# Kernel tuning notes

Measured on AMD Instinct MI355X. Metric: run time of the kernel, lower is better.

Reference implementation:

```python
import jax, jax.numpy as jnp
import numpy as np

N = 100000
E = 1600000
F_IN = 128
H = 128
C = 2


def setup_inputs() -> dict:
    key = jax.random.key(0)
    ks = jax.random.split(key, 12)
    s = lambda fan_in: 1.0 / np.sqrt(fan_in)
    inp = {
        "x": jax.random.normal(ks[0], (N, F_IN), dtype=jnp.float32),
        "edge_index": jax.random.randint(ks[1], (2, E), 0, N, dtype=jnp.int32),
        "edge_weight": jax.random.uniform(ks[2], (E,), dtype=jnp.float32),
        # first_lin: features_num -> hidden
        "W_first": jax.random.uniform(ks[3], (F_IN, H), minval=-s(F_IN), maxval=s(F_IN)),
        "b_first": jnp.zeros((H,), jnp.float32),
        # GRUCell (torch layout: [3*H, H] for ih and hh)
        "W_ih": jax.random.uniform(ks[4], (3 * H, H), minval=-s(H), maxval=s(H)),
        "b_ih": jax.random.uniform(ks[5], (3 * H,), minval=-s(H), maxval=s(H)),
        "W_hh": jax.random.uniform(ks[6], (3 * H, H), minval=-s(H), maxval=s(H)),
        "b_hh": jax.random.uniform(ks[7], (3 * H,), minval=-s(H), maxval=s(H)),
        # lin1: hidden -> hidden
        "W_lin1": jax.random.uniform(ks[8], (H, H), minval=-s(H), maxval=s(H)),
        "b_lin1": jnp.zeros((H,), jnp.float32),
        # out: hidden -> num_class
        "W_out": jax.random.uniform(ks[9], (H, C), minval=-s(H), maxval=s(H)),
        "b_out": jnp.zeros((C,), jnp.float32),
    }
    return inp


def _gated_conv(x, edge_index, edge_weight):
    # gather source node features, scale by edge weight, scatter-add to dst
    src, dst = edge_index[0], edge_index[1]
    msg = x[src] * edge_weight[:, None]           # [E, H]
    return jax.ops.segment_sum(msg, dst, num_segments=N)  # [N, H]


def _gru_cell(inp, hid, W_ih, b_ih, W_hh, b_hh):
    gi = inp @ W_ih.T + b_ih                      # [N, 3H]
    gh = hid @ W_hh.T + b_hh                      # [N, 3H]
    i_r, i_z, i_n = jnp.split(gi, 3, axis=-1)
    h_r, h_z, h_n = jnp.split(gh, 3, axis=-1)
    r = jax.nn.sigmoid(i_r + h_r)
    z = jax.nn.sigmoid(i_z + h_z)
    n = jnp.tanh(i_n + r * h_n)
    return (1.0 - z) * n + z * hid


def reference(x, edge_index, edge_weight, W_first, b_first, W_ih, b_ih,
              W_hh, b_hh, W_lin1, b_lin1, W_out, b_out):
    x = x @ W_first + b_first                     # [N, H] (dropout: eval mode no-op)
    h = x
    x = _gated_conv(x, edge_index, edge_weight)
    x = _gru_cell(x, h, W_ih, b_ih, W_hh, b_hh)
    x = x @ W_lin1 + b_lin1
    x = _gated_conv(x, edge_index, edge_weight)
    x = _gru_cell(x, h, W_ih, b_ih, W_hh, b_hh)
    logits = x @ W_out + b_out                    # [N, C]
    return jax.nn.log_softmax(logits, axis=-1)
```

## Files before the change

### kernel.cpp

```cpp
#include <hip/hip_runtime.h>
#include <hip/hip_bf16.h>

#define H 128
#define SCAN_T 256
#define SCAN_I 8
#define SCAN_CHUNK (SCAN_T * SCAN_I)

typedef __bf16 bf16_t;
typedef __attribute__((ext_vector_type(2))) __bf16 bf16x2;
typedef __attribute__((ext_vector_type(8))) __bf16 bf16x8;
typedef __attribute__((ext_vector_type(4))) float f32x4;

static_assert(sizeof(bf16x8) == 16, "bf16x8 must be 16 bytes");

__device__ inline bf16x8 load_a_frag_f32(const float* __restrict__ A, int row, int koff) {
    const float4* p = (const float4*)(A + (size_t)row * H + koff);
    float4 v0 = p[0], v1 = p[1];
    bf16x8 r;
    r[0] = (bf16_t)v0.x; r[1] = (bf16_t)v0.y; r[2] = (bf16_t)v0.z; r[3] = (bf16_t)v0.w;
    r[4] = (bf16_t)v1.x; r[5] = (bf16_t)v1.y; r[6] = (bf16_t)v1.z; r[7] = (bf16_t)v1.w;
    return r;
}

__global__ void prep_weights(const float* __restrict__ Wf,  const float* __restrict__ Wih,
                             const float* __restrict__ Whh, const float* __restrict__ Wl1,
                             bf16_t* __restrict__ wfT, bf16_t* __restrict__ wih,
                             bf16_t* __restrict__ whh, bf16_t* __restrict__ wl1T) {
    int i = blockIdx.x * blockDim.x + threadIdx.x;
    if (i < 128 * 128) {
        int c = i >> 7, k = i & 127;
        wfT[i]  = (bf16_t)Wf[k * 128 + c];
        wl1T[i] = (bf16_t)Wl1[k * 128 + c];
    }
    if (i < 384 * 128) {
        wih[i] = (bf16_t)Wih[i];
        whh[i] = (bf16_t)Whh[i];
    }
}

__global__ void hist_kernel(const int* __restrict__ ei, int* __restrict__ deg, int nE) {
    int e = blockIdx.x * blockDim.x + threadIdx.x;
    if (e < nE) atomicAdd(&deg[ei[nE + e]], 1);
}

__global__ __launch_bounds__(SCAN_T) void scan1_kernel(
    const int* __restrict__ deg, int* __restrict__ rowptr, int* __restrict__ bsum, int n) {
    __shared__ int s[SCAN_T];
    int base = blockIdx.x * SCAN_CHUNK + threadIdx.x * SCAN_I;
    int v[SCAN_I];
    int sum = 0;
    for (int j = 0; j < SCAN_I; ++j) {
        int idx = base + j;
        v[j] = (idx < n) ? deg[idx] : 0;
        sum += v[j];
    }
    s[threadIdx.x] = sum;
    __syncthreads();
    for (int off = 1; off < SCAN_T; off <<= 1) {
        int t = (threadIdx.x >= off) ? s[threadIdx.x - off] : 0;
        __syncthreads();
        s[threadIdx.x] += t;
        __syncthreads();
    }
    int run = s[threadIdx.x] - sum;
    for (int j = 0; j < SCAN_I; ++j) {
        int idx = base + j;
        if (idx < n) rowptr[idx] = run;
        run += v[j];
    }
    if (threadIdx.x == SCAN_T - 1) bsum[blockIdx.x] = s[SCAN_T - 1];
}

__global__ __launch_bounds__(SCAN_T) void scan2_kernel(int* __restrict__ bsum, int nb) {
    __shared__ int s[SCAN_T];
    int v = (threadIdx.x < nb) ? bsum[threadIdx.x] : 0;
    s[threadIdx.x] = v;
    __syncthreads();
    for (int off = 1; off < SCAN_T; off <<= 1) {
        int t = (threadIdx.x >= off) ? s[threadIdx.x - off] : 0;
        __syncthreads();
        s[threadIdx.x] += t;
        __syncthreads();
    }
    if (threadIdx.x < nb) bsum[threadIdx.x] = s[threadIdx.x] - v;
}

__global__ void scan3_kernel(int* __restrict__ rowptr, int* __restrict__ cursor,
                             const int* __restrict__ bsum, int n, int nE) {
    int idx = blockIdx.x * blockDim.x + threadIdx.x;
    if (idx < n) {
        int val = rowptr[idx] + bsum[idx / SCAN_CHUNK];
        rowptr[idx] = val;
        cursor[idx] = val;
    }
    if (idx == 0) rowptr[n] = nE;
}

__global__ __launch_bounds__(256) void scatter_kernel(
    const int* __restrict__ ei, const float* __restrict__ ew,
    int* __restrict__ cursor, int2* __restrict__ srcw, int nE, int n) {
    int r = blockIdx.x & 7;
    int nslice = n >> 3;
    int lo = r * nslice;
    int hi = (r == 7) ? n : lo + nslice;
    int chunk = blockIdx.x >> 3;
    int nchunk = gridDim.x >> 3;
    for (int e = chunk * 256 + threadIdx.x; e < nE; e += nchunk * 256) {
        int dst = ei[nE + e];
        if (dst >= lo && dst < hi) {
            int pos = atomicAdd(&cursor[dst], 1);
            srcw[pos] = make_int2(ei[e], __float_as_int(ew[e]));
        }
    }
}

__device__ inline void conv_fma(float* acc, uint4 u, float w) {
    acc[0] += __uint_as_float(u.x << 16) * w;
    acc[1] += __uint_as_float(u.x & 0xffff0000u) * w;
    acc[2] += __uint_as_float(u.y << 16) * w;
    acc[3] += __uint_as_float(u.y & 0xffff0000u) * w;
    acc[4] += __uint_as_float(u.z << 16) * w;
    acc[5] += __uint_as_float(u.z & 0xffff0000u) * w;
    acc[6] += __uint_as_float(u.w << 16) * w;
    acc[7] += __uint_as_float(u.w & 0xffff0000u) * w;
}

__global__ __launch_bounds__(256) void conv_csr_kernel(
    const bf16_t* __restrict__ xb, const int* __restrict__ rowptr,
    const int2* __restrict__ srcw, bf16_t* __restrict__ agg, int n) {
    int lane = threadIdx.x & 63;
    int d = (blockIdx.x * blockDim.x + threadIdx.x) >> 6;
    if (d >= n) return;
    int q = lane >> 4;
    int l = lane & 15;
    int beg = rowptr[d], end = rowptr[d + 1];

    float acc[8];
    #pragma unroll
    for (int i = 0; i < 8; ++i) acc[i] = 0.f;

    int e = beg + q;
    for (; e + 4 < end; e += 8) {
        int2 sw0 = srcw[e];
        int2 sw1 = srcw[e + 4];
        uint4 u0 = *(const uint4*)(xb + (size_t)sw0.x * H + l * 8);
        uint4 u1 = *(const uint4*)(xb + (size_t)sw1.x * H + l * 8);
        conv_fma(acc, u0, __int_as_float(sw0.y));
        conv_fma(acc, u1, __int_as_float(sw1.y));
    }
    if (e < end) {
        int2 sw = srcw[e];
        uint4 u = *(const uint4*)(xb + (size_t)sw.x * H + l * 8);
        conv_fma(acc, u, __int_as_float(sw.y));
    }

    #pragma unroll
    for (int i = 0; i < 8; ++i) {
        acc[i] += __shfl_xor(acc[i], 16);
        acc[i] += __shfl_xor(acc[i], 32);
    }
    if (q == 0) {
        bf16x8 r;
        #pragma unroll
        for (int i = 0; i < 8; ++i) r[i] = (bf16_t)acc[i];
        *(bf16x8*)(agg + (size_t)d * H + l * 8) = r;
    }
}


__global__ __launch_bounds__(256) void lin_first_kernel(
    const float* __restrict__ A, const bf16_t* __restrict__ Bt,
    const float* __restrict__ bias, bf16_t* __restrict__ outb, int n) {
    __shared__ __align__(16) unsigned char wlds[32768];
    int tid = threadIdx.x;
    int wid = tid >> 6, lane = tid & 63;
    int r0 = (blockIdx.x * 4 + wid) * 32;
    int lrow = lane & 15, lq = lane >> 4, lk8 = lq * 8;

    #pragma unroll
    for (int i = 0; i < 8; ++i) {
        int g = i * 256 + tid;
        int row = g >> 4, seg = g & 15;
        uint4 v = *(const uint4*)(Bt + row * 128 + seg * 8);
        *(uint4*)(&wlds[row * 256 + ((seg * 16) ^ ((row & 7) << 4))]) = v;
    }

    bf16x8 a[2][4];
    for (int rt = 0; rt < 2; ++rt) {
        int row = r0 + rt * 16 + lrow;
        if (row >= n) row = n - 1;
        for (int t = 0; t < 4; ++t) a[rt][t] = load_a_frag_f32(A, row, t * 32 + lk8);
    }
    __syncthreads();

    for (int ct = 0; ct < 8; ++ct) {
        int c0 = ct * 16;
        f32x4 acc0 = {0.f, 0.f, 0.f, 0.f}, acc1 = {0.f, 0.f, 0.f, 0.f};
        int rbase = (c0 + lrow) * 256;
        int sw = (lrow & 7) << 4;
        #pragma unroll
        for (int t = 0; t < 4; ++t) {
            bf16x8 b = *(const bf16x8*)(&wlds[rbase + ((t * 64 + lq * 16) ^ sw)]);
            acc0 = __builtin_amdgcn_mfma_f32_16x16x32_bf16(a[0][t], b, acc0, 0, 0, 0);
            acc1 = __builtin_amdgcn_mfma_f32_16x16x32_bf16(a[1][t], b, acc1, 0, 0, 0);
        }
        int col = c0 + lrow;
        float bv = bias[col];
        for (int r = 0; r < 4; ++r) {
            int row0 = r0 + lq * 4 + r;
            if (row0 < n) outb[(size_t)row0 * H + col] = (bf16_t)(acc0[r] + bv);
            int row1 = row0 + 16;
            if (row1 < n) outb[(size_t)row1 * H + col] = (bf16_t)(acc1[r] + bv);
        }
    }
}

__global__ __launch_bounds__(256) void lin_mid_kernel(
    const bf16_t* __restrict__ A, const bf16_t* __restrict__ Bt,
    const float* __restrict__ bias, bf16_t* __restrict__ out, int n) {
    __shared__ __align__(16) unsigned char wlds[32768];
    int tid = threadIdx.x;
    int wid = tid >> 6, lane = tid & 63;
    int r0 = (blockIdx.x * 4 + wid) * 32;
    int lrow = lane & 15, lq = lane >> 4, lk8 = lq * 8;

    #pragma unroll
    for (int i = 0; i < 8; ++i) {
        int g = i * 256 + tid;
        int row = g >> 4, seg = g & 15;
        uint4 v = *(const uint4*)(Bt + row * 128 + seg * 8);
        *(uint4*)(&wlds[row * 256 + ((seg * 16) ^ ((row & 7) << 4))]) = v;
    }

    bf16x8 a[2][4];
    for (int rt = 0; rt < 2; ++rt) {
        int row = r0 + rt * 16 + lrow;
        if (row >= n) row = n - 1;
        for (int t = 0; t < 4; ++t)
            a[rt][t] = *(const bf16x8*)(A + (size_t)row * H + t * 32 + lk8);
    }
    __syncthreads();

    for (int ct = 0; ct < 8; ++ct) {
        int c0 = ct * 16;
        f32x4 acc0 = {0.f, 0.f, 0.f, 0.f}, acc1 = {0.f, 0.f, 0.f, 0.f};
        int rbase = (c0 + lrow) * 256;
        int sw = (lrow & 7) << 4;
        #pragma unroll
        for (int t = 0; t < 4; ++t) {
            bf16x8 b = *(const bf16x8*)(&wlds[rbase + ((t * 64 + lq * 16) ^ sw)]);
            acc0 = __builtin_amdgcn_mfma_f32_16x16x32_bf16(a[0][t], b, acc0, 0, 0, 0);
            acc1 = __builtin_amdgcn_mfma_f32_16x16x32_bf16(a[1][t], b, acc1, 0, 0, 0);
        }
        int col = c0 + lrow;
        float bv = bias[col];
        for (int r = 0; r < 4; ++r) {
            int row0 = r0 + lq * 4 + r;
            if (row0 < n) out[(size_t)row0 * H + col] = (bf16_t)(acc0[r] + bv);
            int row1 = row0 + 16;
            if (row1 < n) out[(size_t)row1 * H + col] = (bf16_t)(acc1[r] + bv);
        }
    }
}

template<bool LOGITS>
__global__ __launch_bounds__(256) void gru_kernel(
    const bf16_t* __restrict__ inp, const bf16_t* __restrict__ hidb,
    const bf16_t* __restrict__ Wih, const bf16_t* __restrict__ Whh,
    const float* __restrict__ bih, const float* __restrict__ bhh,
    bf16_t* __restrict__ out, const float* __restrict__ Wo,
    float* __restrict__ pl, int n) {
    __shared__ __align__(16) unsigned char wlds[12 * 4096];
    int tid = threadIdx.x;
    int wid = tid >> 6, lane = tid & 63;
    int cg = blockIdx.x & 3;
    int rb = blockIdx.x >> 2;
    int rstride = gridDim.x >> 2;
    int lrow = lane & 15, lq = lane >> 4, lk8 = lq * 8;

    int srow = tid >> 4, sseg = tid & 15;
    int s_src = srow * 128 + sseg * 8;
    int s_lds = srow * 256 + ((sseg * 16) ^ ((srow & 7) << 4));
    #pragma unroll
    for (int p = 0; p < 2; ++p) {
        #pragma unroll
        for (int s = 0; s < 3; ++s) {
            *(uint4*)(&wlds[(p * 6 + s) * 4096 + s_lds]) =
                *(const uint4*)(Wih + (size_t)(s * 128 + cg * 32 + p * 16) * 128 + s_src);
            *(uint4*)(&wlds[(p * 6 + 3 + s) * 4096 + s_lds]) =
                *(const uint4*)(Whh + (size_t)(s * 128 + cg * 32 + p * 16) * 128 + s_src);
        }
    }
    __syncthreads();

    int colA = cg * 32 + lrow, colB = colA + 16;
    float birA = bih[colA], bizA = bih[128 + colA], binA = bih[256 + colA];
    float bhrA = bhh[colA], bhzA = bhh[128 + colA], bhnA = bhh[256 + colA];
    float birB = bih[colB], bizB = bih[128 + colB], binB = bih[256 + colB];
    float bhrB = bhh[colB], bhzB = bhh[128 + colB], bhnB = bhh[256 + colB];
    float w0A = 0.f, w1A = 0.f, w0B = 0.f, w1B = 0.f;
    if (LOGITS) {
        float2 wa = *(const float2*)(Wo + colA * 2); w0A = wa.x; w1A = wa.y;
        float2 wb = *(const float2*)(Wo + colB * 2); w0B = wb.x; w1B = wb.y;
    }
    bf16x8 bidA, bidB;
    #pragma unroll
    for (int j = 0; j < 8; ++j) {
        bidA[j] = (bf16_t)((lq == (lrow >> 3) && j == (lrow & 7)) ? 1.f : 0.f);
        int ix = 16 + lrow;
        bidB[j] = (bf16_t)((lq == (ix >> 3) && j == (ix & 7)) ? 1.f : 0.f);
    }
    int rbase = lrow * 256;
    int swz = (lrow & 7) << 4;

    int nrt = (n + 63) >> 6;
    for (int rbi = rb; rbi < nrt; rbi += rstride) {
        int r0 = rbi * 64 + wid * 16;
        int rowl = r0 + lrow;
        if (rowl >= n) rowl = n - 1;
        bf16x8 ai[4], ah[4];
        #pragma unroll
        for (int t = 0; t < 4; ++t) {
            ai[t] = *(const bf16x8*)(inp  + (size_t)rowl * H + t * 32 + lk8);
            ah[t] = *(const bf16x8*)(hidb + (size_t)rowl * H + t * 32 + lk8);
        }
        float s0[4], s1[4];
        if (LOGITS) {
            #pragma unroll
            for (int r = 0; r < 4; ++r) { s0[r] = 0.f; s1[r] = 0.f; }
        }

        #pragma unroll
        for (int p = 0; p < 2; ++p) {
            f32x4 air = {0.f,0.f,0.f,0.f}, aiz = {0.f,0.f,0.f,0.f}, ain = {0.f,0.f,0.f,0.f};
            f32x4 ahr = {0.f,0.f,0.f,0.f}, ahz = {0.f,0.f,0.f,0.f}, ahn = {0.f,0.f,0.f,0.f};
            const unsigned char* wb_ = &wlds[p * 6 * 4096];
            #pragma unroll
            for (int t = 0; t < 4; ++t) {
                int roff = rbase + ((t * 64 + lq * 16) ^ swz);
                bf16x8 bir = *(const bf16x8*)(wb_ + 0 * 4096 + roff);
                bf16x8 biz = *(const bf16x8*)(wb_ + 1 * 4096 + roff);
                bf16x8 bin = *(const bf16x8*)(wb_ + 2 * 4096 + roff);
                bf16x8 bhr = *(const bf16x8*)(wb_ + 3 * 4096 + roff);
                bf16x8 bhz = *(const bf16x8*)(wb_ + 4 * 4096 + roff);
                bf16x8 bhn = *(const bf16x8*)(wb_ + 5 * 4096 + roff);
                air = __builtin_amdgcn_mfma_f32_16x16x32_bf16(ai[t], bir, air, 0, 0, 0);
                aiz = __builtin_amdgcn_mfma_f32_16x16x32_bf16(ai[t], biz, aiz, 0, 0, 0);
                ain = __builtin_amdgcn_mfma_f32_16x16x32_bf16(ai[t], bin, ain, 0, 0, 0);
                ahr = __builtin_amdgcn_mfma_f32_16x16x32_bf16(ah[t], bhr, ahr, 0, 0, 0);
                ahz = __builtin_amdgcn_mfma_f32_16x16x32_bf16(ah[t], bhz, ahz, 0, 0, 0);
                ahn = __builtin_amdgcn_mfma_f32_16x16x32_bf16(ah[t], bhn, ahn, 0, 0, 0);
            }
            f32x4 zz = {0.f, 0.f, 0.f, 0.f};
            f32x4 hc = __builtin_amdgcn_mfma_f32_16x16x32_bf16(ah[cg], p ? bidB : bidA, zz, 0, 0, 0);

            float b_ir = p ? birB : birA, b_iz = p ? bizB : bizA, b_in = p ? binB : binA;
            float b_hr = p ? bhrB : bhrA, b_hz = p ? bhzB : bhzA, b_hn = p ? bhnB : bhnA;
            float w0 = p ? w0B : w0A, w1 = p ? w1B : w1A;
            int col = cg * 32 + p * 16 + lrow;
            #pragma unroll
            for (int r = 0; r < 4; ++r) {
                int row = r0 + lq * 4 + r;
                float irv = air[r] + b_ir, hrv = ahr[r] + b_hr;
                float izv = aiz[r] + b_iz, hzv = ahz[r] + b_hz;
                float inv = ain[r] + b_in, hnv = ahn[r] + b_hn;
                float rg = 1.f / (1.f + __expf(-(irv + hrv)));
                float zg = 1.f / (1.f + __expf(-(izv + hzv)));
                float xx = inv + rg * hnv;
                float ng = 2.f / (1.f + __expf(-2.f * xx)) - 1.f;
                float hout = (1.f - zg) * ng + zg * hc[r];
                if (LOGITS) {
                    s0[r] += hout * w0;
                    s1[r] += hout * w1;
                } else if (row < n) {
                    out[(size_t)row * H + col] = (bf16_t)hout;
                }
            }
        }

        if (LOGITS) {
            #pragma unroll
            for (int m = 1; m < 16; m <<= 1) {
                #pragma unroll
                for (int r = 0; r < 4; ++r) {
                    s0[r] += __shfl_xor(s0[r], m);
                    s1[r] += __shfl_xor(s1[r], m);
                }
            }
            if (lrow == 0) {
                #pragma unroll
                for (int r = 0; r < 4; ++r) {
                    int row = r0 + lq * 4 + r;
                    if (row < n) {
                        pl[(size_t)row * 8 + cg * 2]     = s0[r];
                        pl[(size_t)row * 8 + cg * 2 + 1] = s1[r];
                    }
                }
            }
        }
    }
}

__global__ void head_finalize(const float* __restrict__ pl, const float* __restrict__ bo,
                              float* __restrict__ outp, int n) {
    int row = blockIdx.x * blockDim.x + threadIdx.x;
    if (row >= n) return;
    const float4* p = (const float4*)(pl + (size_t)row * 8);
    float4 a = p[0], b = p[1];
    float l0 = a.x + a.z + b.x + b.z + bo[0];
    float l1 = a.y + a.w + b.y + b.w + bo[1];
    float mx = fmaxf(l0, l1);
    float lse = mx + __logf(__expf(l0 - mx) + __expf(l1 - mx));
    outp[(size_t)row * 2]     = l0 - lse;
    outp[(size_t)row * 2 + 1] = l1 - lse;
}

extern "C" void kernel_launch(void* const* d_in, const int* in_sizes, int n_in,
                              void* d_out, int out_size, void* d_ws, size_t ws_size,
                              hipStream_t stream) {
    const float* x   = (const float*)d_in[0];
    const int*   ei  = (const int*)d_in[1];
    const float* ew  = (const float*)d_in[2];
    const float* Wf  = (const float*)d_in[3];
    const float* bf  = (const float*)d_in[4];
    const float* Wih = (const float*)d_in[5];
    const float* bih = (const float*)d_in[6];
    const float* Whh = (const float*)d_in[7];
    const float* bhh = (const float*)d_in[8];
    const float* Wl1 = (const float*)d_in[9];
    const float* bl1 = (const float*)d_in[10];
    const float* Wo  = (const float*)d_in[11];
    const float* bo  = (const float*)d_in[12];

    int n  = in_sizes[0] / H;
    int nE = in_sizes[2];

    bf16_t* hbufb = (bf16_t*)d_ws;
    bf16_t* b1b   = hbufb + (size_t)n * H;
    bf16_t* b2b   = b1b + (size_t)n * H;
    bf16_t* b3b   = b2b + (size_t)n * H;
    float*  pl    = (float*)(b3b + (size_t)n * H);
    bf16_t* wfT   = (bf16_t*)(pl + (size_t)n * 8);
    bf16_t* wih   = wfT + 128 * 128;
    bf16_t* whh   = wih + 384 * 128;
    bf16_t* wl1T  = whh + 384 * 128;
    int* deg    = (int*)(wl1T + 128 * 128);
    int* rowptr = deg + n;
    int* cursor = rowptr + (n + 1);
    int2* srcw  = (int2*)((char*)(cursor + n) + ((size_t)(-(intptr_t)(cursor + n)) & 7));

    int gemmGrid = (n + 127) / 128;
    int nScanBlocks = (n + SCAN_CHUNK - 1) / SCAN_CHUNK;

    prep_weights<<<192, 256, 0, stream>>>(Wf, Wih, Whh, Wl1, wfT, wih, whh, wl1T);
    hipMemsetAsync(deg, 0, (size_t)n * sizeof(int), stream);
    hist_kernel<<<(nE + 255) / 256, 256, 0, stream>>>(ei, deg, nE);
    scan1_kernel<<<nScanBlocks, SCAN_T, 0, stream>>>(deg, rowptr, cursor, n);
    scan2_kernel<<<1, SCAN_T, 0, stream>>>(cursor, nScanBlocks);
    scan3_kernel<<<(n + 255) / 256, 256, 0, stream>>>(rowptr, deg, cursor, n, nE);
    scatter_kernel<<<2048, 256, 0, stream>>>(ei, ew, deg, srcw, nE, n);

    lin_first_kernel<<<gemmGrid, 256, 0, stream>>>(x, wfT, bf, hbufb, n);
    conv_csr_kernel<<<(n + 3) / 4, 256, 0, stream>>>(hbufb, rowptr, srcw, b1b, n);
    gru_kernel<false><<<2048, 256, 0, stream>>>(b1b, hbufb, wih, whh, bih, bhh,
                                                b3b, nullptr, nullptr, n);
    lin_mid_kernel<<<gemmGrid, 256, 0, stream>>>(b3b, wl1T, bl1, b2b, n);
    conv_csr_kernel<<<(n + 3) / 4, 256, 0, stream>>>(b2b, rowptr, srcw, b1b, n);
    gru_kernel<true><<<2048, 256, 0, stream>>>(b1b, hbufb, wih, whh, bih, bhh,
                                               nullptr, Wo, pl, n);
    head_finalize<<<(n + 255) / 256, 256, 0, stream>>>(pl, bo, (float*)d_out, n);
}
```

Before: 583.9 us.

## Double GRU block size to 512 threads, fold biases into accumulators, load hidden directly

The GRU kernel now runs 512-thread blocks (8 waves, 128 rows per tile), so each 48KB LDS weight stage is amortised over twice as many rows, and the grid is halved to keep the same total thread count. Bias values now seed the MFMA accumulators rather than being added after the matmul. The identity-matrix MFMA that extracted the hidden value is replaced by direct bf16 scalar loads from global memory. These changes reduce per-block setup and MFMA work, at the cost of extra scattered 2-byte loads and different register pressure under launch_bounds(512,4).

```diff
diff --git a/kernel.cpp b/kernel.cpp
--- a/kernel.cpp
+++ b/kernel.cpp
@@ -264,7 +264,7 @@
 }
 
 template<bool LOGITS>
-__global__ __launch_bounds__(256) void gru_kernel(
+__global__ __launch_bounds__(512, 4) void gru_kernel(
     const bf16_t* __restrict__ inp, const bf16_t* __restrict__ hidb,
     const bf16_t* __restrict__ Wih, const bf16_t* __restrict__ Whh,
     const float* __restrict__ bih, const float* __restrict__ bhh,
@@ -278,18 +278,19 @@
     int rstride = gridDim.x >> 2;
     int lrow = lane & 15, lq = lane >> 4, lk8 = lq * 8;
 
-    int srow = tid >> 4, sseg = tid & 15;
-    int s_src = srow * 128 + sseg * 8;
-    int s_lds = srow * 256 + ((sseg * 16) ^ ((srow & 7) << 4));
     #pragma unroll
-    for (int p = 0; p < 2; ++p) {
-        #pragma unroll
-        for (int s = 0; s < 3; ++s) {
-            *(uint4*)(&wlds[(p * 6 + s) * 4096 + s_lds]) =
-                *(const uint4*)(Wih + (size_t)(s * 128 + cg * 32 + p * 16) * 128 + s_src);
-            *(uint4*)(&wlds[(p * 6 + 3 + s) * 4096 + s_lds]) =
-                *(const uint4*)(Whh + (size_t)(s * 128 + cg * 32 + p * 16) * 128 + s_src);
-        }
+    for (int i = 0; i < 6; ++i) {
+        int g = i * 512 + tid;
+        int slab = g >> 8;
+        int gi = g & 255;
+        int srow = gi >> 4, sseg = gi & 15;
+        int p = (slab >= 6) ? 1 : 0;
+        int s = slab - p * 6;
+        const bf16_t* base = (s < 3)
+            ? Wih + (size_t)(s * 128 + cg * 32 + p * 16) * 128
+            : Whh + (size_t)((s - 3) * 128 + cg * 32 + p * 16) * 128;
+        uint4 v = *(const uint4*)(base + srow * 128 + sseg * 8);
+        *(uint4*)(&wlds[slab * 4096 + srow * 256 + ((sseg * 16) ^ ((srow & 7) << 4))]) = v;
     }
     __syncthreads();
 
@@ -303,27 +304,35 @@
         float2 wa = *(const float2*)(Wo + colA * 2); w0A = wa.x; w1A = wa.y;
         float2 wb = *(const float2*)(Wo + colB * 2); w0B = wb.x; w1B = wb.y;
     }
-    bf16x8 bidA, bidB;
-    #pragma unroll
-    for (int j = 0; j < 8; ++j) {
-        bidA[j] = (bf16_t)((lq == (lrow >> 3) && j == (lrow & 7)) ? 1.f : 0.f);
-        int ix = 16 + lrow;
-        bidB[j] = (bf16_t)((lq == (ix >> 3) && j == (ix & 7)) ? 1.f : 0.f);
-    }
     int rbase = lrow * 256;
     int swz = (lrow & 7) << 4;
 
-    int nrt = (n + 63) >> 6;
+    int nrt = (n + 127) >> 7;
     for (int rbi = rb; rbi < nrt; rbi += rstride) {
-        int r0 = rbi * 64 + wid * 16;
+        int r0 = rbi * 128 + wid * 16;
         int rowl = r0 + lrow;
         if (rowl >= n) rowl = n - 1;
+
         bf16x8 ai[4], ah[4];
         #pragma unroll
         for (int t = 0; t < 4; ++t) {
             ai[t] = *(const bf16x8*)(inp  + (size_t)rowl * H + t * 32 + lk8);
             ah[t] = *(const bf16x8*)(hidb + (size_t)rowl * H + t * 32 + lk8);
         }
+        int rc0 = r0 + lq * 4;
+        int c0 = (rc0     < n ? rc0     : n - 1);
+        int c1 = (rc0 + 1 < n ? rc0 + 1 : n - 1);
+        int c2 = (rc0 + 2 < n ? rc0 + 2 : n - 1);
+        int c3 = (rc0 + 3 < n ? rc0 + 3 : n - 1);
+        unsigned short ha0 = *(const unsigned short*)(hidb + (size_t)c0 * H + colA);
+        unsigned short ha1 = *(const unsigned short*)(hidb + (size_t)c1 * H + colA);
+        unsigned short ha2 = *(const unsigned short*)(hidb + (size_t)c2 * H + colA);
+        unsigned short ha3 = *(const unsigned short*)(hidb + (size_t)c3 * H + colA);
+        unsigned short hb0 = *(const unsigned short*)(hidb + (size_t)c0 * H + colB);
+        unsigned short hb1 = *(const unsigned short*)(hidb + (size_t)c1 * H + colB);
+        unsigned short hb2 = *(const unsigned short*)(hidb + (size_t)c2 * H + colB);
+        unsigned short hb3 = *(const unsigned short*)(hidb + (size_t)c3 * H + colB);
+
         float s0[4], s1[4];
         if (LOGITS) {
             #pragma unroll
@@ -332,8 +341,11 @@
 
         #pragma unroll
         for (int p = 0; p < 2; ++p) {
-            f32x4 air = {0.f,0.f,0.f,0.f}, aiz = {0.f,0.f,0.f,0.f}, ain = {0.f,0.f,0.f,0.f};
-            f32x4 ahr = {0.f,0.f,0.f,0.f}, ahz = {0.f,0.f,0.f,0.f}, ahn = {0.f,0.f,0.f,0.f};
+            float b_ir = p ? birB : birA, b_iz = p ? bizB : bizA, b_in = p ? binB : binA;
+            float b_hr = p ? bhrB : bhrA, b_hz = p ? bhzB : bhzA, b_hn = p ? bhnB : bhnA;
+            f32x4 air = {b_ir, b_ir, b_ir, b_ir}, aiz = {b_iz, b_iz, b_iz, b_iz},
+                  ain = {b_in, b_in, b_in, b_in}, ahr = {b_hr, b_hr, b_hr, b_hr},
+                  ahz = {b_hz, b_hz, b_hz, b_hz}, ahn = {b_hn, b_hn, b_hn, b_hn};
             const unsigned char* wb_ = &wlds[p * 6 * 4096];
             #pragma unroll
             for (int t = 0; t < 4; ++t) {
@@ -351,24 +363,20 @@
                 ahz = __builtin_amdgcn_mfma_f32_16x16x32_bf16(ah[t], bhz, ahz, 0, 0, 0);
                 ahn = __builtin_amdgcn_mfma_f32_16x16x32_bf16(ah[t], bhn, ahn, 0, 0, 0);
             }
-            f32x4 zz = {0.f, 0.f, 0.f, 0.f};
-            f32x4 hc = __builtin_amdgcn_mfma_f32_16x16x32_bf16(ah[cg], p ? bidB : bidA, zz, 0, 0, 0);
-
-            float b_ir = p ? birB : birA, b_iz = p ? bizB : bizA, b_in = p ? binB : binA;
-            float b_hr = p ? bhrB : bhrA, b_hz = p ? bhzB : bhzA, b_hn = p ? bhnB : bhnA;
+
             float w0 = p ? w0B : w0A, w1 = p ? w1B : w1A;
             int col = cg * 32 + p * 16 + lrow;
             #pragma unroll
             for (int r = 0; r < 4; ++r) {
                 int row = r0 + lq * 4 + r;
-                float irv = air[r] + b_ir, hrv = ahr[r] + b_hr;
-                float izv = aiz[r] + b_iz, hzv = ahz[r] + b_hz;
-                float inv = ain[r] + b_in, hnv = ahn[r] + b_hn;
-                float rg = 1.f / (1.f + __expf(-(irv + hrv)));
-                float zg = 1.f / (1.f + __expf(-(izv + hzv)));
-                float xx = inv + rg * hnv;
+                unsigned short hu = p ? (r == 0 ? hb0 : r == 1 ? hb1 : r == 2 ? hb2 : hb3)
+                                      : (r == 0 ? ha0 : r == 1 ? ha1 : r == 2 ? ha2 : ha3);
+                float hv = __uint_as_float((unsigned)hu << 16);
+                float rg = 1.f / (1.f + __expf(-(air[r] + ahr[r])));
+                float zg = 1.f / (1.f + __expf(-(aiz[r] + ahz[r])));
+                float xx = ain[r] + rg * ahn[r];
                 float ng = 2.f / (1.f + __expf(-2.f * xx)) - 1.f;
-                float hout = (1.f - zg) * ng + zg * hc[r];
+                float hout = (1.f - zg) * ng + zg * hv;
                 if (LOGITS) {
                     s0[r] += hout * w0;
                     s1[r] += hout * w1;
@@ -462,11 +470,11 @@
 
     lin_first_kernel<<<gemmGrid, 256, 0, stream>>>(x, wfT, bf, hbufb, n);
     conv_csr_kernel<<<(n + 3) / 4, 256, 0, stream>>>(hbufb, rowptr, srcw, b1b, n);
-    gru_kernel<false><<<2048, 256, 0, stream>>>(b1b, hbufb, wih, whh, bih, bhh,
+    gru_kernel<false><<<1024, 512, 0, stream>>>(b1b, hbufb, wih, whh, bih, bhh,
                                                 b3b, nullptr, nullptr, n);
     lin_mid_kernel<<<gemmGrid, 256, 0, stream>>>(b3b, wl1T, bl1, b2b, n);
     conv_csr_kernel<<<(n + 3) / 4, 256, 0, stream>>>(b2b, rowptr, srcw, b1b, n);
-    gru_kernel<true><<<2048, 256, 0, stream>>>(b1b, hbufb, wih, whh, bih, bhh,
+    gru_kernel<true><<<1024, 512, 0, stream>>>(b1b, hbufb, wih, whh, bih, bhh,
                                                nullptr, Wo, pl, n);
     head_finalize<<<(n + 255) / 256, 256, 0, stream>>>(pl, bo, (float*)d_out, n);
 }
```

New measurement: 1.057 ms. 81.1% more time.

## Precompute shared hidden-state GRU projection once and reuse across both GRU steps

Applied to the files above, without the earlier changes.

Both GRU cells use the same hidden state h, so h@W_hh^T+b_hh is computed once in a new gh_kernel and stored as bf16 [N,384]. The GRU kernels then do only the input-side MFMAs and read the precomputed gates, halving their matmul work and LDS weight footprint. In exchange it adds an extra kernel plus writing and reading roughly 77MB of gh data with uncoalesced 2-byte loads, and rounds the hidden gate values to bf16.

```diff
diff --git a/kernel.cpp b/kernel.cpp
--- a/kernel.cpp
+++ b/kernel.cpp
@@ -167,7 +167,6 @@
     }
 }
 
-
 __global__ __launch_bounds__(256) void lin_first_kernel(
     const float* __restrict__ A, const bf16_t* __restrict__ Bt,
     const float* __restrict__ bias, bf16_t* __restrict__ outb, int n) {
@@ -263,14 +262,10 @@
     }
 }
 
-template<bool LOGITS>
-__global__ __launch_bounds__(256) void gru_kernel(
-    const bf16_t* __restrict__ inp, const bf16_t* __restrict__ hidb,
-    const bf16_t* __restrict__ Wih, const bf16_t* __restrict__ Whh,
-    const float* __restrict__ bih, const float* __restrict__ bhh,
-    bf16_t* __restrict__ out, const float* __restrict__ Wo,
-    float* __restrict__ pl, int n) {
-    __shared__ __align__(16) unsigned char wlds[12 * 4096];
+__global__ __launch_bounds__(256) void gh_kernel(
+    const bf16_t* __restrict__ hidb, const bf16_t* __restrict__ Whh,
+    const float* __restrict__ bhh, bf16_t* __restrict__ ghb, int n) {
+    __shared__ __align__(16) unsigned char wlds[6 * 4096];
     int tid = threadIdx.x;
     int wid = tid >> 6, lane = tid & 63;
     int cg = blockIdx.x & 3;
@@ -278,38 +273,23 @@
     int rstride = gridDim.x >> 2;
     int lrow = lane & 15, lq = lane >> 4, lk8 = lq * 8;
 
-    int srow = tid >> 4, sseg = tid & 15;
-    int s_src = srow * 128 + sseg * 8;
-    int s_lds = srow * 256 + ((sseg * 16) ^ ((srow & 7) << 4));
     #pragma unroll
-    for (int p = 0; p < 2; ++p) {
-        #pragma unroll
-        for (int s = 0; s < 3; ++s) {
-            *(uint4*)(&wlds[(p * 6 + s) * 4096 + s_lds]) =
-                *(const uint4*)(Wih + (size_t)(s * 128 + cg * 32 + p * 16) * 128 + s_src);
-            *(uint4*)(&wlds[(p * 6 + 3 + s) * 4096 + s_lds]) =
-                *(const uint4*)(Whh + (size_t)(s * 128 + cg * 32 + p * 16) * 128 + s_src);
-        }
+    for (int i = 0; i < 6; ++i) {
+        int g = i * 256 + tid;
+        int slab = g >> 8;
+        int gi = g & 255;
+        int srow = gi >> 4, sseg = gi & 15;
+        int p = (slab >= 3) ? 1 : 0;
+        int s = slab - p * 3;
+        const bf16_t* base = Whh + (size_t)(s * 128 + cg * 32 + p * 16) * 128;
+        uint4 v = *(const uint4*)(base + srow * 128 + sseg * 8);
+        *(uint4*)(&wlds[slab * 4096 + srow * 256 + ((sseg * 16) ^ ((srow & 7) << 4))]) = v;
     }
     __syncthreads();
 
     int colA = cg * 32 + lrow, colB = colA + 16;
-    float birA = bih[colA], bizA = bih[128 + colA], binA = bih[256 + colA];
-    float bhrA = bhh[colA], bhzA = bhh[128 + colA], bhnA = bhh[256 + colA];
-    float birB = bih[colB], bizB = bih[128 + colB], binB = bih[256 + colB];
-    float bhrB = bhh[colB], bhzB = bhh[128 + colB], bhnB = bhh[256 + colB];
-    float w0A = 0.f, w1A = 0.f, w0B = 0.f, w1B = 0.f;
-    if (LOGITS) {
-        float2 wa = *(const float2*)(Wo + colA * 2); w0A = wa.x; w1A = wa.y;
-        float2 wb = *(const float2*)(Wo + colB * 2); w0B = wb.x; w1B = wb.y;
-    }
-    bf16x8 bidA, bidB;
-    #pragma unroll
-    for (int j = 0; j < 8; ++j) {
-        bidA[j] = (bf16_t)((lq == (lrow >> 3) && j == (lrow & 7)) ? 1.f : 0.f);
-        int ix = 16 + lrow;
-        bidB[j] = (bf16_t)((lq == (ix >> 3) && j == (ix & 7)) ? 1.f : 0.f);
-    }
+    float bA0 = bhh[colA], bA1 = bhh[128 + colA], bA2 = bhh[256 + colA];
+    float bB0 = bhh[colB], bB1 = bhh[128 + colB], bB2 = bhh[256 + colB];
     int rbase = lrow * 256;
     int swz = (lrow & 7) << 4;
 
@@ -318,12 +298,90 @@
         int r0 = rbi * 64 + wid * 16;
         int rowl = r0 + lrow;
         if (rowl >= n) rowl = n - 1;
-        bf16x8 ai[4], ah[4];
-        #pragma unroll
-        for (int t = 0; t < 4; ++t) {
-            ai[t] = *(const bf16x8*)(inp  + (size_t)rowl * H + t * 32 + lk8);
+        bf16x8 ah[4];
+        #pragma unroll
+        for (int t = 0; t < 4; ++t)
             ah[t] = *(const bf16x8*)(hidb + (size_t)rowl * H + t * 32 + lk8);
-        }
+
+        #pragma unroll
+        for (int p = 0; p < 2; ++p) {
+            float b0 = p ? bB0 : bA0, b1 = p ? bB1 : bA1, b2 = p ? bB2 : bA2;
+            f32x4 a0 = {b0, b0, b0, b0}, a1 = {b1, b1, b1, b1}, a2 = {b2, b2, b2, b2};
+            const unsigned char* wb_ = &wlds[p * 3 * 4096];
+            #pragma unroll
+            for (int t = 0; t < 4; ++t) {
+                int roff = rbase + ((t * 64 + lq * 16) ^ swz);
+                bf16x8 w0 = *(const bf16x8*)(wb_ + 0 * 4096 + roff);
+                bf16x8 w1 = *(const bf16x8*)(wb_ + 1 * 4096 + roff);
+                bf16x8 w2 = *(const bf16x8*)(wb_ + 2 * 4096 + roff);
+                a0 = __builtin_amdgcn_mfma_f32_16x16x32_bf16(ah[t], w0, a0, 0, 0, 0);
+                a1 = __builtin_amdgcn_mfma_f32_16x16x32_bf16(ah[t], w1, a1, 0, 0, 0);
+                a2 = __builtin_amdgcn_mfma_f32_16x16x32_bf16(ah[t], w2, a2, 0, 0, 0);
+            }
+            int col = cg * 32 + p * 16 + lrow;
+            #pragma unroll
+            for (int r = 0; r < 4; ++r) {
+                int row = r0 + lq * 4 + r;
+                if (row < n) {
+                    ghb[(size_t)row * 384 +       col] = (bf16_t)a0[r];
+                    ghb[(size_t)row * 384 + 128 + col] = (bf16_t)a1[r];
+                    ghb[(size_t)row * 384 + 256 + col] = (bf16_t)a2[r];
+                }
+            }
+        }
+    }
+}
+
+template<bool LOGITS>
+__global__ void gru_kernel(
+    const bf16_t* __restrict__ inp, const bf16_t* __restrict__ hidb,
+    const bf16_t* __restrict__ ghb,
+    const bf16_t* __restrict__ Wih, const float* __restrict__ bih,
+    bf16_t* __restrict__ out, const float* __restrict__ Wo,
+    float* __restrict__ pl, int n) {
+    __shared__ __align__(16) unsigned char wlds[6 * 4096];
+    int tid = threadIdx.x;
+    int wid = tid >> 6, lane = tid & 63;
+    int cg = blockIdx.x & 3;
+    int rb = blockIdx.x >> 2;
+    int rstride = gridDim.x >> 2;
+    int lrow = lane & 15, lq = lane >> 4, lk8 = lq * 8;
+
+    #pragma unroll
+    for (int i = 0; i < 6; ++i) {
+        int g = i * 256 + tid;
+        int slab = g >> 8;
+        int gi = g & 255;
+        int srow = gi >> 4, sseg = gi & 15;
+        int p = (slab >= 3) ? 1 : 0;
+        int s = slab - p * 3;
+        const bf16_t* base = Wih + (size_t)(s * 128 + cg * 32 + p * 16) * 128;
+        uint4 v = *(const uint4*)(base + srow * 128 + sseg * 8);
+        *(uint4*)(&wlds[slab * 4096 + srow * 256 + ((sseg * 16) ^ ((srow & 7) << 4))]) = v;
+    }
+    __syncthreads();
+
+    int colA = cg * 32 + lrow, colB = colA + 16;
+    float bA0 = bih[colA], bA1 = bih[128 + colA], bA2 = bih[256 + colA];
+    float bB0 = bih[colB], bB1 = bih[128 + colB], bB2 = bih[256 + colB];
+    float w0A = 0.f, w1A = 0.f, w0B = 0.f, w1B = 0.f;
+    if (LOGITS) {
+        float2 wa = *(const float2*)(Wo + colA * 2); w0A = wa.x; w1A = wa.y;
+        float2 wb = *(const float2*)(Wo + colB * 2); w0B = wb.x; w1B = wb.y;
+    }
+    int rbase = lrow * 256;
+    int swz = (lrow & 7) << 4;
+
+    int nrt = (n + 63) >> 6;
+    for (int rbi = rb; rbi < nrt; rbi += rstride) {
+        int r0 = rbi * 64 + wid * 16;
+        int rowl = r0 + lrow;
+        if (rowl >= n) rowl = n - 1;
+        bf16x8 ai[4];
+        #pragma unroll
+        for (int t = 0; t < 4; ++t)
+            ai[t] = *(const bf16x8*)(inp + (size_t)rowl * H + t * 32 + lk8);
+
         float s0[4], s1[4];
         if (LOGITS) {
             #pragma unroll
@@ -332,43 +390,46 @@
 
         #pragma unroll
         for (int p = 0; p < 2; ++p) {
-            f32x4 air = {0.f,0.f,0.f,0.f}, aiz = {0.f,0.f,0.f,0.f}, ain = {0.f,0.f,0.f,0.f};
-            f32x4 ahr = {0.f,0.f,0.f,0.f}, ahz = {0.f,0.f,0.f,0.f}, ahn = {0.f,0.f,0.f,0.f};
-            const unsigned char* wb_ = &wlds[p * 6 * 4096];
+            int col = cg * 32 + p * 16 + lrow;
+            unsigned short ghr[4], ghz[4], ghn[4], hs[4];
+            #pragma unroll
+            for (int r = 0; r < 4; ++r) {
+                int row = r0 + lq * 4 + r;
+                if (row >= n) row = n - 1;
+                const bf16_t* gp = ghb + (size_t)row * 384 + col;
+                ghr[r] = *(const unsigned short*)(gp);
+                ghz[r] = *(const unsigned short*)(gp + 128);
+                ghn[r] = *(const unsigned short*)(gp + 256);
+                hs[r]  = *(const unsigned short*)(hidb + (size_t)row * H + col);
+            }
+
+            float b0 = p ? bB0 : bA0, b1 = p ? bB1 : bA1, b2 = p ? bB2 : bA2;
+            f32x4 aR = {b0, b0, b0, b0}, aZ = {b1, b1, b1, b1}, aN = {b2, b2, b2, b2};
+            const unsigned char* wb_ = &wlds[p * 3 * 4096];
             #pragma unroll
             for (int t = 0; t < 4; ++t) {
                 int roff = rbase + ((t * 64 + lq * 16) ^ swz);
-                bf16x8 bir = *(const bf16x8*)(wb_ + 0 * 4096 + roff);
-                bf16x8 biz = *(const bf16x8*)(wb_ + 1 * 4096 + roff);
-                bf16x8 bin = *(const bf16x8*)(wb_ + 2 * 4096 + roff);
-                bf16x8 bhr = *(const bf16x8*)(wb_ + 3 * 4096 + roff);
-                bf16x8 bhz = *(const bf16x8*)(wb_ + 4 * 4096 + roff);
-                bf16x8 bhn = *(const bf16x8*)(wb_ + 5 * 4096 + roff);
-                air = __builtin_amdgcn_mfma_f32_16x16x32_bf16(ai[t], bir, air, 0, 0, 0);
-                aiz = __builtin_amdgcn_mfma_f32_16x16x32_bf16(ai[t], biz, aiz, 0, 0, 0);
-                ain = __builtin_amdgcn_mfma_f32_16x16x32_bf16(ai[t], bin, ain, 0, 0, 0);
-                ahr = __builtin_amdgcn_mfma_f32_16x16x32_bf16(ah[t], bhr, ahr, 0, 0, 0);
-                ahz = __builtin_amdgcn_mfma_f32_16x16x32_bf16(ah[t], bhz, ahz, 0, 0, 0);
-                ahn = __builtin_amdgcn_mfma_f32_16x16x32_bf16(ah[t], bhn, ahn, 0, 0, 0);
-            }
-            f32x4 zz = {0.f, 0.f, 0.f, 0.f};
-            f32x4 hc = __builtin_amdgcn_mfma_f32_16x16x32_bf16(ah[cg], p ? bidB : bidA, zz, 0, 0, 0);
-
-            float b_ir = p ? birB : birA, b_iz = p ? bizB : bizA, b_in = p ? binB : binA;
-            float b_hr = p ? bhrB : bhrA, b_hz = p ? bhzB : bhzA, b_hn = p ? bhnB : bhnA;
+                bf16x8 wR = *(const bf16x8*)(wb_ + 0 * 4096 + roff);
+                bf16x8 wZ = *(const bf16x8*)(wb_ + 1 * 4096 + roff);
+                bf16x8 wN = *(const bf16x8*)(wb_ + 2 * 4096 + roff);
+                aR = __builtin_amdgcn_mfma_f32_16x16x32_bf16(ai[t], wR, aR, 0, 0, 0);
+                aZ = __builtin_amdgcn_mfma_f32_16x16x32_bf16(ai[t], wZ, aZ, 0, 0, 0);
+                aN = __builtin_amdgcn_mfma_f32_16x16x32_bf16(ai[t], wN, aN, 0, 0, 0);
+            }
+
             float w0 = p ? w0B : w0A, w1 = p ? w1B : w1A;
-            int col = cg * 32 + p * 16 + lrow;
             #pragma unroll
             for (int r = 0; r < 4; ++r) {
                 int row = r0 + lq * 4 + r;
-                float irv = air[r] + b_ir, hrv = ahr[r] + b_hr;
-                float izv = aiz[r] + b_iz, hzv = ahz[r] + b_hz;
-                float inv = ain[r] + b_in, hnv = ahn[r] + b_hn;
-                float rg = 1.f / (1.f + __expf(-(irv + hrv)));
-                float zg = 1.f / (1.f + __expf(-(izv + hzv)));
-                float xx = inv + rg * hnv;
+                float gr = __uint_as_float((unsigned)ghr[r] << 16);
+                float gz = __uint_as_float((unsigned)ghz[r] << 16);
+                float gn = __uint_as_float((unsigned)ghn[r] << 16);
+                float hv = __uint_as_float((unsigned)hs[r] << 16);
+                float rg = 1.f / (1.f + __expf(-(aR[r] + gr)));
+                float zg = 1.f / (1.f + __expf(-(aZ[r] + gz)));
+                float xx = aN[r] + rg * gn;
                 float ng = 2.f / (1.f + __expf(-2.f * xx)) - 1.f;
-                float hout = (1.f - zg) * ng + zg * hc[r];
+                float hout = (1.f - zg) * ng + zg * hv;
                 if (LOGITS) {
                     s0[r] += hout * w0;
                     s1[r] += hout * w1;
@@ -439,8 +500,8 @@
     bf16_t* b1b   = hbufb + (size_t)n * H;
     bf16_t* b2b   = b1b + (size_t)n * H;
     bf16_t* b3b   = b2b + (size_t)n * H;
-    float*  pl    = (float*)(b3b + (size_t)n * H);
-    bf16_t* wfT   = (bf16_t*)(pl + (size_t)n * 8);
+    bf16_t* ghb   = b3b + (size_t)n * H;
+    bf16_t* wfT   = ghb + (size_t)n * 384;
     bf16_t* wih   = wfT + 128 * 128;
     bf16_t* whh   = wih + 384 * 128;
     bf16_t* wl1T  = whh + 384 * 128;
@@ -448,6 +509,7 @@
     int* rowptr = deg + n;
     int* cursor = rowptr + (n + 1);
     int2* srcw  = (int2*)((char*)(cursor + n) + ((size_t)(-(intptr_t)(cursor + n)) & 7));
+    float* pl   = (float*)b2b;
 
     int gemmGrid = (n + 127) / 128;
     int nScanBlocks = (n + SCAN_CHUNK - 1) / SCAN_CHUNK;
@@ -461,12 +523,13 @@
     scatter_kernel<<<2048, 256, 0, stream>>>(ei, ew, deg, srcw, nE, n);
 
     lin_first_kernel<<<gemmGrid, 256, 0, stream>>>(x, wfT, bf, hbufb, n);
+    gh_kernel<<<2048, 256, 0, stream>>>(hbufb, whh, bhh, ghb, n);
     conv_csr_kernel<<<(n + 3) / 4, 256, 0, stream>>>(hbufb, rowptr, srcw, b1b, n);
-    gru_kernel<false><<<2048, 256, 0, stream>>>(b1b, hbufb, wih, whh, bih, bhh,
+    gru_kernel<false><<<2048, 256, 0, stream>>>(b1b, hbufb, ghb, wih, bih,
                                                 b3b, nullptr, nullptr, n);
     lin_mid_kernel<<<gemmGrid, 256, 0, stream>>>(b3b, wl1T, bl1, b2b, n);
     conv_csr_kernel<<<(n + 3) / 4, 256, 0, stream>>>(b2b, rowptr, srcw, b1b, n);
-    gru_kernel<true><<<2048, 256, 0, stream>>>(b1b, hbufb, wih, whh, bih, bhh,
+    gru_kernel<true><<<2048, 256, 0, stream>>>(b1b, hbufb, ghb, wih, bih,
                                                nullptr, Wo, pl, n);
     head_finalize<<<(n + 255) / 256, 256, 0, stream>>>(pl, bo, (float*)d_out, n);
 }
```

After: 652.9 us. 11.8% more time.
